# Optimization experiments

Hardware: AMD Instinct MI355X
Metric: run time of the kernel (lower is better)

The kernel has to match this reference:

```python
import jax, jax.numpy as jnp
import numpy as np

B, T, D_IN, H, C = 1024, 85, 20, 1024, 27
OBJ = T * 36  # flattened (T, 12, 3) object stream


def _mlp(h, W1, b1, W2, b2):
    # BaseEncoderDecoderLayout stand-in: Dense(H, relu) -> Dense(out)
    return jnp.maximum(h @ W1 + b1, 0.0) @ W2 + b2


def setup_inputs() -> dict:
    key = jax.random.key(0)
    ks = jax.random.split(key, 8)
    s = lambda k, shape: jax.random.normal(k, shape, jnp.float32) * 0.02
    return {
        "o": jax.random.normal(ks[0], (B, OBJ), jnp.float32),
        "x": jax.random.normal(ks[1], (B, T, D_IN), jnp.float32),
        # objProcess = BaseEncoderDecoderLayout(num_hid, dim_output=num_hid)
        "oW1": s(ks[2], (OBJ, H)), "ob1": jnp.zeros((H,), jnp.float32),
        "oW2": s(ks[3], (H, H)), "ob2": jnp.zeros((H,), jnp.float32),
        # expertWeightNet = BaseEncoderDecoderLayout(num_hid, dim_output=num_classes)
        "eW1": s(ks[4], (D_IN + H, H)), "eb1": jnp.zeros((H,), jnp.float32),
        "eW2": s(ks[5], (H, C)), "eb2": jnp.zeros((C,), jnp.float32),
    }


def reference(o, x, oW1, ob1, oW2, ob2, eW1, eb1, eW2, eb2):
    objInfo = _mlp(o, oW1, ob1, oW2, ob2)  # [B, H]

    def expert(cur):  # cur: [B, D_IN]
        return _mlp(jnp.concatenate([cur, objInfo], axis=-1), eW1, eb1, eW2, eb2)

    # step 0 uses raw x[:, 0, :]
    ew0 = expert(x[:, 0, :])  # [B, C]

    # steps 1..T-2: first feature of currentInput is replaced by previous
    # result's channel-0, i.e. result[:, -1, 0] -> sequential recurrence
    def step(prev, xt):  # prev: [B], xt: [B, D_IN]
        cur = jnp.concatenate([prev[:, None], xt[:, 1:]], axis=-1)
        ew = expert(cur)
        return ew[:, 0], ew

    xs = jnp.swapaxes(x[:, 1:T - 1, :], 0, 1)  # [T-2, B, D_IN]
    _, rest = jax.lax.scan(step, ew0[:, 0], xs)  # rest: [T-2, B, C]

    result = jnp.concatenate([ew0[None], rest], axis=0)  # [T-1, B, C]
    return jnp.swapaxes(result, 0, 1)  # [B, T-1, C]
```

## Files before the change

### kernel.cpp

```cpp
#include <hip/hip_runtime.h>
#include <hip/hip_bf16.h>

#define B_   1024
#define T_   85
#define DIN  20
#define H_   1024
#define C_   27
#define OBJ_ (T_ * 36)
#define TOUT (T_ - 1)

typedef unsigned short u16;
typedef __attribute__((ext_vector_type(8))) short bf16x8;
typedef __attribute__((ext_vector_type(4))) float f32x4;

__device__ __forceinline__ u16 f2bf(float f) {
    __hip_bfloat16 h = __float2bfloat16(f);
    return *reinterpret_cast<u16*>(&h);
}
__device__ __forceinline__ float bf2f(u16 u) {
    __hip_bfloat16 h;
    *reinterpret_cast<u16*>(&h) = u;
    return __bfloat162float(h);
}
__device__ __forceinline__ int f_as_i(float f) {
    union { float f; int i; } u; u.f = f; return u.i;
}
__device__ __forceinline__ float i_as_f(int i) {
    union { float f; int i; } u; u.i = i; return u.f;
}

__device__ __forceinline__ float wave64_sum_bcast(float p) {
    p += i_as_f(__builtin_amdgcn_update_dpp(0, f_as_i(p), 0x111, 0xf, 0xf, true));
    p += i_as_f(__builtin_amdgcn_update_dpp(0, f_as_i(p), 0x112, 0xf, 0xf, true));
    p += i_as_f(__builtin_amdgcn_update_dpp(0, f_as_i(p), 0x114, 0xf, 0xf, true));
    p += i_as_f(__builtin_amdgcn_update_dpp(0, f_as_i(p), 0x118, 0xf, 0xf, true));
    p += i_as_f(__builtin_amdgcn_update_dpp(0, f_as_i(p), 0x142, 0xa, 0xf, true));
    p += i_as_f(__builtin_amdgcn_update_dpp(0, f_as_i(p), 0x143, 0xc, 0xf, true));
    return i_as_f(__builtin_amdgcn_readlane(f_as_i(p), 63));
}

__global__ __launch_bounds__(256) void convertK2(
    const float* __restrict__ o, const float* __restrict__ oW1,
    const float* __restrict__ eW1, const float* __restrict__ oW2,
    const float* __restrict__ eW2, const float* __restrict__ ob2,
    u16* __restrict__ o_bf, u16* __restrict__ bW1t, u16* __restrict__ bE1t,
    u16* __restrict__ o2bf, u16* __restrict__ w2th,
    u16* __restrict__ e1t20, float* __restrict__ biasp)
{
    __shared__ float tl[64][65];
    const int bid = blockIdx.x, t = threadIdx.x;

    if (bid < 512) {
        for (int it = 0; it < 6; ++it) {
            const int idx = (bid * 256 + t) + it * 131072;
            const int row = idx / 768, g = idx - row * 768;
            float4 v = make_float4(0.f, 0.f, 0.f, 0.f);
            if (g < 765) v = *(const float4*)(o + (size_t)row * 3060 + g * 4);
            const float* vp = (const float*)&v;
            ushort4 uh;
            uh.x = f2bf(vp[0]); uh.y = f2bf(vp[1]);
            uh.z = f2bf(vp[2]); uh.w = f2bf(vp[3]);
            *(ushort4*)(o_bf + (size_t)row * 3072 + g * 4) = uh;
        }
    } else if (bid < 1536) {
        const bool isW1 = (bid < 1280);
        const int idx = isW1 ? (bid - 512) : (bid - 1280);
        const int k0 = (idx >> 4) * 64, n0 = (idx & 15) * 64;
        const float* src = isW1 ? oW1 : (eW1 + (size_t)DIN * H_);
        const int Ksrc = isW1 ? 3060 : 1024;
        u16* dst = isW1 ? bW1t : bE1t;
        const int ldk = isW1 ? 3072 : 1024;
#pragma unroll
        for (int r = 0; r < 4; ++r) {
            const int k = k0 + r * 16 + (t >> 4);
            float4 v = make_float4(0.f, 0.f, 0.f, 0.f);
            if (k < Ksrc)
                v = *(const float4*)(src + (size_t)k * 1024 + n0 + (t & 15) * 4);
            const float* vp = (const float*)&v;
#pragma unroll
            for (int j = 0; j < 4; ++j)
                tl[r * 16 + (t >> 4)][(t & 15) * 4 + j] = vp[j];
        }
        __syncthreads();
#pragma unroll
        for (int r = 0; r < 4; ++r) {
            const int n = r * 16 + (t >> 4);
            ushort4 u;
            u.x = f2bf(tl[(t & 15) * 4 + 0][n]);
            u.y = f2bf(tl[(t & 15) * 4 + 1][n]);
            u.z = f2bf(tl[(t & 15) * 4 + 2][n]);
            u.w = f2bf(tl[(t & 15) * 4 + 3][n]);
            *(ushort4*)(dst + (size_t)(n0 + n) * ldk + k0 + (t & 15) * 4) = u;
        }
    } else if (bid < 1664) {
        const int base = (bid - 1536) * 256 + t;
#pragma unroll
        for (int it = 0; it < 8; ++it) {
            const int g = base + it * 32768;
            float4 v = *(const float4*)(oW2 + (size_t)g * 4);
            const float* vp = (const float*)&v;
            ushort4 uh;
            uh.x = f2bf(vp[0]); uh.y = f2bf(vp[1]);
            uh.z = f2bf(vp[2]); uh.w = f2bf(vp[3]);
            *(ushort4*)(o2bf + (size_t)g * 4) = uh;
        }
    } else if (bid < 1696) {
        const int c = bid - 1664;
#pragma unroll
        for (int kk = 0; kk < 4; ++kk) {
            const int k = kk * 256 + t;
            const float v = (c < C_) ? eW2[(size_t)k * C_ + c] : 0.f;
            w2th[(size_t)c * 1024 + k] = f2bf(v);
        }
    } else if (bid < 1700) {
        const int n = (bid - 1696) * 256 + t;
        u16 buf[32];
#pragma unroll
        for (int k = 0; k < 32; ++k)
            buf[k] = (k < DIN) ? f2bf(eW1[(size_t)k * H_ + n]) : (u16)0;
#pragma unroll
        for (int q = 0; q < 4; ++q)
            *(uint4*)(e1t20 + (size_t)n * 32 + q * 8) = *(uint4*)&buf[q * 8];
    } else {
        const int r = bid - 1700, kc = r >> 2, nb = r & 3;
        const int n = nb * 256 + t;
        const int k0 = kc * 128;
        float acc = 0.f;
#pragma unroll 8
        for (int k = 0; k < 128; ++k)
            acc = fmaf(ob2[k0 + k], eW1[(size_t)(DIN + k0 + k) * H_ + n], acc);
        biasp[kc * H_ + n] = acc;
    }
}

template <int BN>
__device__ __forceinline__ void gemm_mfma_tile(
    const u16* __restrict__ A0, const u16* __restrict__ Bt,
    float* __restrict__ C, const float* __restrict__ bias,
    int ldK, int nk1, int gm0, int gn0, char* lds)
{
    constexpr int FN    = BN / 32;
    constexpr int WNw   = BN / 2;
    constexpr int BR    = BN / 64;
    constexpr int BUFSZ = 8192 + BN * 64;

    const int tid  = threadIdx.x;
    const int wave = tid >> 6, l = tid & 63, ml = l & 15, koct = l >> 4;
    const int wm = wave >> 1, wn = wave & 1;
    const int swz = koct ^ ((ml >> 1) & 3);
    const int a_ro = (wm * 64 + ml) * 64 + swz * 16;
    const int b_ro = (wn * WNw + ml) * 64 + swz * 16;

    const int sm = tid >> 2, sq = tid & 3;
    int wAo[2], wBo[BR];
    size_t gAo[2], gBo[BR];
#pragma unroll
    for (int q = 0; q < 2; ++q) {
        const int m = q * 64 + sm;
        wAo[q] = m * 64 + ((sq ^ ((m >> 1) & 3)) * 16);
        gAo[q] = (size_t)(gm0 + m) * ldK * 2 + sq * 16;
    }
#pragma unroll
    for (int q = 0; q < BR; ++q) {
        const int n = q * 64 + sm;
        wBo[q] = n * 64 + ((sq ^ ((n >> 1) & 3)) * 16);
        gBo[q] = (size_t)(gn0 + n) * ldK * 2 + sq * 16;
    }

    f32x4 acc[4][FN];
    const f32x4 zz = {0.f, 0.f, 0.f, 0.f};
#pragma unroll
    for (int i = 0; i < 4; ++i)
#pragma unroll
        for (int j = 0; j < FN; ++j) acc[i][j] = zz;

    const char* A0c = (const char*)A0;
    const char* Btc = (const char*)Bt;

    uint4 st[2 + BR];
    auto stage = [&](int kt) {
        const size_t koff = (size_t)kt * 64;
        st[0] = *(const uint4*)(A0c + gAo[0] + koff);
        st[1] = *(const uint4*)(A0c + gAo[1] + koff);
#pragma unroll
        for (int q = 0; q < BR; ++q)
            st[2 + q] = *(const uint4*)(Btc + gBo[q] + koff);
    };
    auto dswrite = [&](int buf) {
        char* d = lds + buf * BUFSZ;
        *(uint4*)(d + wAo[0]) = st[0];
        *(uint4*)(d + wAo[1]) = st[1];
#pragma unroll
        for (int q = 0; q < BR; ++q)
            *(uint4*)(d + 8192 + wBo[q]) = st[2 + q];
    };
    auto compute = [&](int buf) {
        const char* As = lds + buf * BUFSZ;
        const char* Bs = As + 8192;
        bf16x8 af[4], bfv[FN];
#pragma unroll
        for (int fm = 0; fm < 4; ++fm)
            af[fm] = *(const bf16x8*)(As + a_ro + fm * 1024);
#pragma unroll
        for (int fn = 0; fn < FN; ++fn)
            bfv[fn] = *(const bf16x8*)(Bs + b_ro + fn * 1024);
#pragma unroll
        for (int fm = 0; fm < 4; ++fm)
#pragma unroll
            for (int fn = 0; fn < FN; ++fn)
                acc[fm][fn] = __builtin_amdgcn_mfma_f32_16x16x32_bf16(
                    af[fm], bfv[fn], acc[fm][fn], 0, 0, 0);
    };

    stage(0); dswrite(0); __syncthreads();
    for (int kt = 0; kt < nk1; ++kt) {
        if (kt + 1 < nk1) stage(kt + 1);
        compute(kt & 1);
        if (kt + 1 < nk1) dswrite((kt + 1) & 1);
        __syncthreads();
    }

    float br[FN];
#pragma unroll
    for (int fn = 0; fn < FN; ++fn)
        br[fn] = bias ? bias[gn0 + wn * WNw + fn * 16 + ml] : 0.f;
#pragma unroll
    for (int fm = 0; fm < 4; ++fm) {
        const int rowb = gm0 + wm * 64 + fm * 16 + koct * 4;
#pragma unroll
        for (int fn = 0; fn < FN; ++fn) {
            const int col = gn0 + wn * WNw + fn * 16 + ml;
#pragma unroll
            for (int r = 0; r < 4; ++r)
                C[(size_t)(rowb + r) * 1024 + col] = acc[fm][fn][r] + br[fn];
        }
    }
}

__global__ __launch_bounds__(256) void kernelA2(
    const u16* __restrict__ o_bf, const u16* __restrict__ bW1t,
    const u16* __restrict__ o2bf, const u16* __restrict__ bE1t,
    float* __restrict__ p_h1, float* __restrict__ p_wc)
{
    __shared__ alignas(16) char lds[2 * 12288];
    const int bid = blockIdx.x;
    if (bid < 384) {
        const int c = bid >> 7, tl = bid & 127;
        gemm_mfma_tile<64>(o_bf + c * 1024, bW1t + c * 1024,
                           p_h1 + (size_t)c * 1048576, nullptr, 3072, 32,
                           (tl >> 4) * 128, (tl & 15) * 64, lds);
    } else {
        const int tl = bid - 384;
        gemm_mfma_tile<64>(o2bf, bE1t, p_wc, nullptr, 1024, 32,
                           (tl >> 4) * 128, (tl & 15) * 64, lds);
    }
}

__global__ __launch_bounds__(256) void epilogue2(
    const float* __restrict__ p_h1, const float* __restrict__ p_wc,
    const float* __restrict__ ob1, const float* __restrict__ eb1,
    const float* __restrict__ biasp,
    u16* __restrict__ h1bf, u16* __restrict__ Wct, float* __restrict__ biasWc)
{
    __shared__ float tl[64][65];
    const int bid = blockIdx.x, t = threadIdx.x;
    if (bid < 256) {
#pragma unroll
        for (int it = 0; it < 4; ++it) {
            const int g = bid * 1024 + it * 256 + t;
            const size_t e = (size_t)g * 4;
            float4 a = *(const float4*)(p_h1 + e);
            float4 b = *(const float4*)(p_h1 + 1048576 + e);
            float4 c = *(const float4*)(p_h1 + 2097152 + e);
            float4 s = *(const float4*)(ob1 + (e & 1023));
            const float *ap = (const float*)&a, *bp = (const float*)&b,
                        *cp = (const float*)&c, *sp = (const float*)&s;
            ushort4 uh;
            u16* up = (u16*)&uh;
#pragma unroll
            for (int j = 0; j < 4; ++j)
                up[j] = f2bf(fmaxf(ap[j] + bp[j] + cp[j] + sp[j], 0.f));
            *(ushort4*)(h1bf + e) = uh;
        }
    } else if (bid < 512) {
        const int idx = bid - 256;
        const int k0 = (idx >> 4) * 64, n0 = (idx & 15) * 64;
#pragma unroll
        for (int r = 0; r < 4; ++r) {
            const int k = k0 + r * 16 + (t >> 4);
            float4 v = *(const float4*)(p_wc + (size_t)k * 1024 + n0 + (t & 15) * 4);
            const float* vp = (const float*)&v;
#pragma unroll
            for (int j = 0; j < 4; ++j)
                tl[r * 16 + (t >> 4)][(t & 15) * 4 + j] = vp[j];
        }
        __syncthreads();
#pragma unroll
        for (int r = 0; r < 4; ++r) {
            const int n = r * 16 + (t >> 4);
            ushort4 u;
            u.x = f2bf(tl[(t & 15) * 4 + 0][n]);
            u.y = f2bf(tl[(t & 15) * 4 + 1][n]);
            u.z = f2bf(tl[(t & 15) * 4 + 2][n]);
            u.w = f2bf(tl[(t & 15) * 4 + 3][n]);
            *(ushort4*)(Wct + (size_t)(n0 + n) * 1024 + k0 + (t & 15) * 4) = u;
        }
    } else {
        const int j0 = t * 4;
        float4 s = *(const float4*)(eb1 + j0);
        float* sp = (float*)&s;
#pragma unroll
        for (int kc = 0; kc < 8; ++kc) {
            float4 p = *(const float4*)(biasp + kc * H_ + j0);
            const float* pp = (const float*)&p;
#pragma unroll
            for (int i = 0; i < 4; ++i) sp[i] += pp[i];
        }
        *(float4*)(biasWc + j0) = s;
    }
}

__global__ __launch_bounds__(256) void kernelB2(
    const u16* __restrict__ h1bf, const u16* __restrict__ Wct,
    const float* __restrict__ biasWc,
    float* __restrict__ base0, float* __restrict__ base1)
{
    __shared__ alignas(16) char lds[2 * 12288];
    const int bid = blockIdx.x;
    const int p = bid >> 7, tl = bid & 127;
    gemm_mfma_tile<64>(h1bf + p * 512, Wct + p * 512,
                       p ? base1 : base0, p ? biasWc : nullptr,
                       1024, 16, (tl >> 4) * 128, (tl & 15) * 64, lds);
}

#define CPH 16
#define CNPH 6

__global__ __launch_bounds__(64) void chain_seq4(
    const float* __restrict__ x, const u16* __restrict__ e1t20,
    const float* __restrict__ eW1, const float* __restrict__ eW2,
    const float* __restrict__ eb2,
    const float* __restrict__ base0, const float* __restrict__ base1,
    float* __restrict__ cur0_buf)
{
    __shared__ u16   A_bf[CPH * 1032];
    __shared__ float base_s[1024];
    __shared__ u16   xstage[16 * 32];

    const int b = blockIdx.x, l = threadIdx.x;
    const int ml = l & 15, koct = l >> 4;

#pragma unroll
    for (int i = 0; i < 16; ++i) {
        const int j = i * 64 + l;
        base_s[j] = base0[(size_t)b * H_ + j] + base1[(size_t)b * H_ + j];
    }
    float u[16], v[16];
#pragma unroll
    for (int i = 0; i < 16; ++i) {
        const int j = i * 64 + l;
        u[i] = eW1[j];
        v[i] = eW2[(size_t)j * C_];
    }
    const float eb20 = eb2[0];
    const float cur0_init = x[(size_t)b * (T_ * DIN)];
    float* cb = cur0_buf + (size_t)b * TOUT;

    const f32x4 zz = {0.f, 0.f, 0.f, 0.f};
    float prev = 0.f;
    int t = 0;

#pragma unroll 1
    for (int ph = 0; ph < CNPH; ++ph) {
        const int t0 = ph * CPH;

        {
            const int tr = l >> 2, kq = l & 3;
            const int tg = t0 + tr;
            u16 hw[8];
#pragma unroll
            for (int e = 0; e < 8; ++e) {
                const int k = kq * 8 + e;
                float vx = 0.f;
                if (k >= 1 && k < DIN && tg < T_)
                    vx = x[(size_t)b * (T_ * DIN) + tg * DIN + k];
                hw[e] = f2bf(vx);
            }
            uint4 pk;
            pk.x = hw[0] | ((unsigned)hw[1] << 16);
            pk.y = hw[2] | ((unsigned)hw[3] << 16);
            pk.z = hw[4] | ((unsigned)hw[5] << 16);
            pk.w = hw[6] | ((unsigned)hw[7] << 16);
            *(uint4*)&xstage[tr * 32 + kq * 8] = pk;
        }
        __syncthreads();

        {
            const bf16x8 af = *(const bf16x8*)&xstage[ml * 32 + koct * 8];
#pragma unroll 4
            for (int jt = 0; jt < 64; ++jt) {
                const bf16x8 bf = *(const bf16x8*)
                    &e1t20[(size_t)(jt * 16 + ml) * 32 + koct * 8];
                f32x4 c = __builtin_amdgcn_mfma_f32_16x16x32_bf16(
                    af, bf, zz, 0, 0, 0);
                const int jcol = jt * 16 + ml;
                const float bj = base_s[jcol];
#pragma unroll
                for (int r = 0; r < 4; ++r)
                    A_bf[(koct * 4 + r) * 1032 + jcol] = f2bf(c[r] + bj);
            }
        }
        __syncthreads();

        const int rem = 83 - t0;
        const int nst = (rem < CPH) ? rem : CPH;

        float a_cur[16];
#pragma unroll
        for (int i = 0; i < 16; ++i)
            a_cur[i] = bf2f(A_bf[i * 64 + l]);

        for (int sl = 0; sl < nst; ++sl, ++t) {
            const int sln = (sl + 1 < nst) ? sl + 1 : sl;
            float a_nxt[16];
#pragma unroll
            for (int i = 0; i < 16; ++i)
                a_nxt[i] = bf2f(A_bf[sln * 1032 + i * 64 + l]);

            const float cur0 = (t == 0) ? cur0_init : prev;
            if (l == 0) cb[t] = cur0;

            float p0 = 0.f, p1 = 0.f, p2 = 0.f, p3 = 0.f;
#pragma unroll
            for (int i = 0; i < 16; i += 4) {
                p0 = fmaf(fmaxf(fmaf(cur0, u[i + 0], a_cur[i + 0]), 0.f), v[i + 0], p0);
                p1 = fmaf(fmaxf(fmaf(cur0, u[i + 1], a_cur[i + 1]), 0.f), v[i + 1], p1);
                p2 = fmaf(fmaxf(fmaf(cur0, u[i + 2], a_cur[i + 2]), 0.f), v[i + 2], p2);
                p3 = fmaf(fmaxf(fmaf(cur0, u[i + 3], a_cur[i + 3]), 0.f), v[i + 3], p3);
            }
            const float p = (p0 + p1) + (p2 + p3);
            prev = eb20 + wave64_sum_bcast(p);

#pragma unroll
            for (int i = 0; i < 16; ++i) a_cur[i] = a_nxt[i];
        }
        __syncthreads();
    }
    if (l == 0) cb[TOUT - 1] = prev;
}

__global__ __launch_bounds__(256, 4) void expand(
    const float* __restrict__ x, const float* __restrict__ base0,
    const float* __restrict__ base1, const float* __restrict__ cur0_buf,
    const u16* __restrict__ e1t20, const u16* __restrict__ w2th,
    const float* __restrict__ eb2, float* __restrict__ out)
{
    __shared__ u16 A_lds[64 * 32];
    __shared__ u16 e_lds[128 * 32];
    __shared__ u16 h_lds[64 * 128];
    __shared__ u16 w2_s[32 * 128];
    __shared__ float base_s[2 * 128];

    const int tid = threadIdx.x;
    const int g0 = blockIdx.x * 64;
    const int w = tid >> 6, l = tid & 63, ml = l & 15, koct = l >> 4;
    const int b0 = g0 / 84;
    const int b1 = (b0 + 1 < B_) ? b0 + 1 : b0;

    {
        const int row = tid >> 2, q = tid & 3;
        const int g = g0 + row, bb = g / 84, tt = g - bb * 84;
        u16 hw[8];
#pragma unroll
        for (int c = 0; c < 8; ++c) {
            const int k = q * 8 + c;
            float v = 0.f;
            if (k == 0) v = cur0_buf[g];
            else if (k < DIN) v = x[(size_t)bb * (T_ * DIN) + tt * DIN + k];
            hw[c] = f2bf(v);
        }
        uint4 pk;
        pk.x = hw[0] | ((unsigned)hw[1] << 16);
        pk.y = hw[2] | ((unsigned)hw[3] << 16);
        pk.z = hw[4] | ((unsigned)hw[5] << 16);
        pk.w = hw[6] | ((unsigned)hw[7] << 16);
        *(uint4*)&A_lds[row * 32 + q * 8] = pk;
    }

    const int grow = w * 16 + ml;
    const int g = g0 + grow;
    const int sel = g / 84 - b0;
    __syncthreads();
    const bf16x8 xfrag = *(const bf16x8*)&A_lds[grow * 32 + koct * 8];

    f32x4 acc[2];
    const f32x4 zz = {0.f, 0.f, 0.f, 0.f};
    acc[0] = zz; acc[1] = zz;

#pragma unroll 1
    for (int kc = 0; kc < 8; ++kc) {
        const int n0 = kc * 128;
        if (kc) __syncthreads();
        {
            const u16* src = e1t20 + n0 * 32 + tid * 16;
            *(uint4*)&e_lds[tid * 16]     = *(const uint4*)src;
            *(uint4*)&e_lds[tid * 16 + 8] = *(const uint4*)(src + 8);
        }
        {
            const int wr = tid >> 3, sg = tid & 7;
            const u16* srcw = w2th + (size_t)wr * 1024 + n0 + sg * 16;
            const int s0 = (sg * 2) ^ (wr & 15), s1 = (sg * 2 + 1) ^ (wr & 15);
            *(uint4*)&w2_s[wr * 128 + s0 * 8] = *(const uint4*)srcw;
            *(uint4*)&w2_s[wr * 128 + s1 * 8] = *(const uint4*)(srcw + 8);
        }
        {
            const int bs = tid >> 7, c = tid & 127;
            const size_t rb = (size_t)(bs ? b1 : b0) * H_ + n0 + c;
            base_s[bs * 128 + c] = base0[rb] + base1[rb];
        }
        __syncthreads();

#pragma unroll
        for (int p = 0; p < 8; ++p) {
            const bf16x8 ef = *(const bf16x8*)&e_lds[(p * 16 + ml) * 32 + koct * 8];
            f32x4 c1 = zz;
            c1 = __builtin_amdgcn_mfma_f32_16x16x32_bf16(ef, xfrag, c1, 0, 0, 0);
            u16 hq[4];
#pragma unroll
            for (int q = 0; q < 4; ++q) {
                const int j = p * 16 + koct * 4 + q;
                const float v = c1[q] + base_s[sel * 128 + j];
                hq[q] = f2bf(fmaxf(v, 0.f));
            }
            uint2 pk;
            pk.x = hq[0] | ((unsigned)hq[1] << 16);
            pk.y = hq[2] | ((unsigned)hq[3] << 16);
            const int s16 = (p * 2 + (koct >> 1)) ^ ml;
            *(uint2*)&h_lds[grow * 128 + s16 * 8 + (koct & 1) * 4] = pk;
        }

#pragma unroll
        for (int ks = 0; ks < 4; ++ks) {
            const int sl = (((ks * 4 + koct) ^ ml)) * 8;
            const bf16x8 hf = *(const bf16x8*)&h_lds[grow * 128 + sl];
#pragma unroll
            for (int ct = 0; ct < 2; ++ct) {
                const bf16x8 wf = *(const bf16x8*)&w2_s[(ct * 16 + ml) * 128 + sl];
                acc[ct] = __builtin_amdgcn_mfma_f32_16x16x32_bf16(
                    wf, hf, acc[ct], 0, 0, 0);
            }
        }
    }

#pragma unroll
    for (int ct = 0; ct < 2; ++ct) {
#pragma unroll
        for (int q = 0; q < 4; ++q) {
            const int c = ct * 16 + koct * 4 + q;
            if (c < C_)
                out[(size_t)g * C_ + c] = acc[ct][q] + eb2[c];
        }
    }
}

struct GemmSmem {
    float As[2][16][68];
    float Bs[2][16][64];
};

template <int RELU>
__device__ __forceinline__ void gemm_core(
    const float* __restrict__ A, int lda,
    const float* __restrict__ Bm, int ldb,
    const float* __restrict__ bias, const float* __restrict__ bias_parts,
    float* __restrict__ Cc, int ldc, int K, int tile, GemmSmem& sm)
{
    const int tid = threadIdx.x;
    const int bm = (tile >> 4) * 64, bn = (tile & 15) * 64;
    const int wave = tid >> 6, l = tid & 63;
    const int n0 = (wave & 1) * 32 + (l & 7) * 4;
    const int m0 = (wave >> 1) * 32 + (l >> 3) * 4;
    const int am = tid >> 2, akq = tid & 3;
    const int bk = tid >> 4, bnq = tid & 15;
    const float* Arow = A + (size_t)(bm + am) * lda + akq * 4;
    const float* Brow = Bm + (size_t)bk * ldb + bn + bnq * 4;
    float acc[4][4] = {};
    const int nIter = (K + 15) >> 4;
    {
        const int ak = akq * 4;
        float4 av = (ak + 4 <= K) ? *(const float4*)(Arow)
                                  : make_float4(0.f, 0.f, 0.f, 0.f);
        float4 bv = (bk < K) ? *(const float4*)(Brow)
                             : make_float4(0.f, 0.f, 0.f, 0.f);
        sm.As[0][akq * 4 + 0][am] = av.x; sm.As[0][akq * 4 + 1][am] = av.y;
        sm.As[0][akq * 4 + 2][am] = av.z; sm.As[0][akq * 4 + 3][am] = av.w;
        *(float4*)&sm.Bs[0][bk][bnq * 4] = bv;
    }
    __syncthreads();
    for (int it = 0; it < nIter; ++it) {
        const int cur = it & 1;
        const bool pf = (it + 1 < nIter);
        float4 pav, pbv;
        if (pf) {
            const int k0 = (it + 1) << 4, ak = k0 + akq * 4;
            pav = (ak + 4 <= K) ? *(const float4*)(Arow + k0)
                                : make_float4(0.f, 0.f, 0.f, 0.f);
            pbv = (k0 + bk < K) ? *(const float4*)(Brow + (size_t)k0 * ldb)
                                : make_float4(0.f, 0.f, 0.f, 0.f);
        }
#pragma unroll
        for (int kk = 0; kk < 16; ++kk) {
            float ar[4], br[4];
            *(float4*)ar = *(const float4*)&sm.As[cur][kk][m0];
            *(float4*)br = *(const float4*)&sm.Bs[cur][kk][n0];
#pragma unroll
            for (int r = 0; r < 4; ++r)
#pragma unroll
                for (int c = 0; c < 4; ++c)
                    acc[r][c] = fmaf(ar[r], br[c], acc[r][c]);
        }
        if (pf) {
            const int nb = cur ^ 1;
            sm.As[nb][akq * 4 + 0][am] = pav.x; sm.As[nb][akq * 4 + 1][am] = pav.y;
            sm.As[nb][akq * 4 + 2][am] = pav.z; sm.As[nb][akq * 4 + 3][am] = pav.w;
            *(float4*)&sm.Bs[nb][bk][bnq * 4] = pbv;
        }
        __syncthreads();
    }
    float bias4[4];
#pragma unroll
    for (int c = 0; c < 4; ++c) {
        const int col = bn + n0 + c;
        float b = bias ? bias[col] : 0.f;
        if (bias_parts)
#pragma unroll
            for (int p = 0; p < 8; ++p) b += bias_parts[p * H_ + col];
        bias4[c] = b;
    }
#pragma unroll
    for (int r = 0; r < 4; ++r) {
        float4 v; float* vp = (float*)&v;
#pragma unroll
        for (int c = 0; c < 4; ++c) {
            float t2 = acc[r][c] + bias4[c];
            if (RELU) t2 = fmaxf(t2, 0.f);
            vp[c] = t2;
        }
        *(float4*)&Cc[(size_t)(bm + m0 + r) * ldc + bn + n0] = v;
    }
}

__global__ __launch_bounds__(256) void kernelA_fb(
    const float* __restrict__ o, const float* __restrict__ oW1,
    const float* __restrict__ ob1, const float* __restrict__ oW2,
    const float* __restrict__ eW1, const float* __restrict__ ob2,
    float* __restrict__ h1, float* __restrict__ Wc, float* __restrict__ biasc)
{
    __shared__ GemmSmem sm;
    const int bid = blockIdx.x;
    if (bid < 256) {
        gemm_core<1>(o, OBJ_, oW1, H_, ob1, nullptr, h1, H_, OBJ_, bid, sm);
    } else if (bid < 512) {
        gemm_core<0>(oW2, H_, eW1 + (size_t)DIN * H_, H_, nullptr, nullptr,
                     Wc, H_, H_, bid - 256, sm);
    } else {
        const int r = bid - 512, kc = r >> 2, nb = r & 3;
        const int n = nb * 256 + (int)threadIdx.x;
        const int k0 = kc * 128;
        float acc = 0.f;
#pragma unroll 8
        for (int k = 0; k < 128; ++k)
            acc = fmaf(ob2[k0 + k], eW1[(size_t)(DIN + k0 + k) * H_ + n], acc);
        biasc[kc * H_ + n] = acc;
    }
}

__global__ __launch_bounds__(256) void kernelB_fb(
    const float* __restrict__ h1, const float* __restrict__ Wc,
    const float* __restrict__ eb1, const float* __restrict__ biasc,
    float* __restrict__ base0)
{
    __shared__ GemmSmem sm;
    gemm_core<0>(h1, H_, Wc, H_, eb1, biasc, base0, H_, H_, blockIdx.x, sm);
}

__global__ __launch_bounds__(256, 2) void expert_seq_fb(
    const float* __restrict__ x, const float* __restrict__ eW1,
    const float* __restrict__ eW2, const float* __restrict__ eb2,
    const float* __restrict__ base0, float* __restrict__ out)
{
    const int b   = blockIdx.x;
    const int tid = threadIdx.x;
    const int j0  = tid * 4;

    __shared__ float xl[T_ * DIN];
    __shared__ float pl[256 * 29];
    __shared__ float pl2[256];
    __shared__ float prevs;

    for (int idx = tid; idx < T_ * DIN; idx += 256)
        xl[idx] = x[(size_t)b * (T_ * DIN) + idx];

    float w1r[DIN][4];
#pragma unroll
    for (int d = 0; d < DIN; ++d)
        *(float4*)w1r[d] = *(const float4*)&eW1[(size_t)d * H_ + j0];

    float base_r[4];
    *(float4*)base_r = *(const float4*)&base0[(size_t)b * H_ + j0];

    float w2r[4][C_];
#pragma unroll
    for (int i = 0; i < 4; ++i)
#pragma unroll
        for (int c = 0; c < C_; ++c)
            w2r[i][c] = eW2[(size_t)(j0 + i) * C_ + c];

    const float myb = (tid < C_) ? eb2[tid] : 0.f;
    __syncthreads();

    float prev = 0.f;
#pragma unroll 1
    for (int t = 0; t < TOUT; ++t) {
        const float cur0 = (t == 0) ? xl[0] : prev;
        float h[4];
#pragma unroll
        for (int i = 0; i < 4; ++i)
            h[i] = fmaf(cur0, w1r[0][i], base_r[i]);
#pragma unroll
        for (int d = 1; d < DIN; ++d) {
            const float xv = xl[t * DIN + d];
#pragma unroll
            for (int i = 0; i < 4; ++i)
                h[i] = fmaf(xv, w1r[d][i], h[i]);
        }
#pragma unroll
        for (int i = 0; i < 4; ++i)
            h[i] = fmaxf(h[i], 0.f);
        float p[C_];
#pragma unroll
        for (int c = 0; c < C_; ++c)
            p[c] = h[0] * w2r[0][c];
#pragma unroll
        for (int i = 1; i < 4; ++i)
#pragma unroll
            for (int c = 0; c < C_; ++c)
                p[c] = fmaf(h[i], w2r[i][c], p[c]);
#pragma unroll
        for (int c = 0; c < C_; ++c)
            pl[tid * 29 + c] = p[c];
        __syncthreads();
        {
            const int c2 = tid & 31, grp = tid >> 5;
            float s = 0.f;
            if (c2 < C_) {
                const int basei = grp * 32 * 29 + c2;
#pragma unroll
                for (int s2 = 0; s2 < 32; ++s2)
                    s += pl[basei + s2 * 29];
            }
            pl2[tid] = s;
        }
        __syncthreads();
        if (tid < C_) {
            float o = myb;
#pragma unroll
            for (int g = 0; g < 8; ++g)
                o += pl2[g * 32 + tid];
            out[((size_t)b * TOUT + t) * C_ + tid] = o;
            if (tid == 0) prevs = o;
        }
        __syncthreads();
        prev = prevs;
    }
}

extern "C" void kernel_launch(void* const* d_in, const int* in_sizes, int n_in,
                              void* d_out, int out_size, void* d_ws, size_t ws_size,
                              hipStream_t stream)
{
    const float* o   = (const float*)d_in[0];
    const float* x   = (const float*)d_in[1];
    const float* oW1 = (const float*)d_in[2];
    const float* ob1 = (const float*)d_in[3];
    const float* oW2 = (const float*)d_in[4];
    const float* ob2 = (const float*)d_in[5];
    const float* eW1 = (const float*)d_in[6];
    const float* eb1 = (const float*)d_in[7];
    const float* eW2 = (const float*)d_in[8];
    const float* eb2 = (const float*)d_in[9];

    float* outp = (float*)d_out;
    float* ws   = (float*)d_ws;
    dim3 blk(256);

    const size_t NEED2 = 38326272;
    if (ws_size >= NEED2) {
        float* p_h1   = ws;
        float* p_wc   = ws + 3145728;
        float* biasWc = ws + 4194304;
        float* cur0b  = ws + 4195328;
        float* biasp  = ws + 4281344;
        u16*   ub     = (u16*)(ws + 4289536);
        u16 *o_bf  = ub,             *bW1t = ub + 3145728;
        u16 *bE1t  = ub + 6291456,   *o2bf = ub + 7340032;
        u16 *h1bf  = ub + 8388608,   *Wct  = ub + 9437184;
        u16 *w2th  = ub + 10485760;
        u16 *e1t20 = ub + 10551296;
        float* base0 = p_h1;
        float* base1 = p_h1 + 1048576;

        convertK2<<<dim3(1732), blk, 0, stream>>>(o, oW1, eW1, oW2, eW2, ob2,
                                                  o_bf, bW1t, bE1t, o2bf,
                                                  w2th, e1t20, biasp);
        kernelA2<<<dim3(512), blk, 0, stream>>>(o_bf, bW1t, o2bf, bE1t,
                                                p_h1, p_wc);
        epilogue2<<<dim3(513), blk, 0, stream>>>(p_h1, p_wc, ob1, eb1, biasp,
                                                 h1bf, Wct, biasWc);
        kernelB2<<<dim3(256), blk, 0, stream>>>(h1bf, Wct, biasWc,
                                                base0, base1);
        chain_seq4<<<dim3(B_), dim3(64), 0, stream>>>(x, e1t20, eW1, eW2, eb2,
                                                      base0, base1, cur0b);
        expand<<<dim3(1344), blk, 0, stream>>>(x, base0, base1, cur0b, e1t20,
                                               w2th, eb2, outp);
    } else {
        const size_t MF = (size_t)H_ * H_;
        float* h1    = ws;
        float* Wc    = ws + MF;
        float* base0 = ws + 2 * MF;
        float* biasc = outp;
        kernelA_fb<<<dim3(544), blk, 0, stream>>>(o, oW1, ob1, oW2, eW1, ob2,
                                                  h1, Wc, biasc);
        kernelB_fb<<<dim3(256), blk, 0, stream>>>(h1, Wc, eb1, biasc, base0);
        expert_seq_fb<<<dim3(B_), blk, 0, stream>>>(x, eW1, eW2, eb2,
                                                    base0, outp);
    }
}
```

Before: 166.1 us.

## Warp-specialize chain kernel: producer waves precompute next phase while one wave runs recurrence

The sequential chain kernel now runs 256 threads per block. Three producer waves compute the MFMA pre-activations for the next phase of 8 steps into a double-buffered LDS tile, while wave 0 runs the serial recurrence on the current phase. This hides the per-phase MFMA prologue behind the latency-bound recurrence. The costs are more barriers (11 phases instead of 6), a larger LDS footprint and block size that may lower occupancy, and producer work wasted on lanes whose output is discarded.

Result: no change. 165.7 us (-0.3%).

```diff
diff --git a/kernel.cpp b/kernel.cpp
--- a/kernel.cpp
+++ b/kernel.cpp
@@ -333,120 +333,138 @@
                        1024, 16, (tl >> 4) * 128, (tl & 15) * 64, lds);
 }
 
-#define CPH 16
-#define CNPH 6
-
-__global__ __launch_bounds__(64) void chain_seq4(
+#define CPH 8
+#define CNPH 11
+
+__global__ __launch_bounds__(256, 3) void chain_seq5(
     const float* __restrict__ x, const u16* __restrict__ e1t20,
     const float* __restrict__ eW1, const float* __restrict__ eW2,
     const float* __restrict__ eb2,
     const float* __restrict__ base0, const float* __restrict__ base1,
     float* __restrict__ cur0_buf)
 {
-    __shared__ u16   A_bf[CPH * 1032];
+    __shared__ u16   A_bf[2][CPH * 1032];
     __shared__ float base_s[1024];
-    __shared__ u16   xstage[16 * 32];
-
-    const int b = blockIdx.x, l = threadIdx.x;
+
+    const int b = blockIdx.x, tid = threadIdx.x;
+    const int w = tid >> 6, l = tid & 63;
     const int ml = l & 15, koct = l >> 4;
 
-#pragma unroll
-    for (int i = 0; i < 16; ++i) {
-        const int j = i * 64 + l;
-        base_s[j] = base0[(size_t)b * H_ + j] + base1[(size_t)b * H_ + j];
-    }
-    float u[16], v[16];
-#pragma unroll
-    for (int i = 0; i < 16; ++i) {
-        const int j = i * 64 + l;
-        u[i] = eW1[j];
-        v[i] = eW2[(size_t)j * C_];
-    }
-    const float eb20 = eb2[0];
-    const float cur0_init = x[(size_t)b * (T_ * DIN)];
-    float* cb = cur0_buf + (size_t)b * TOUT;
+    {
+        const int j = tid * 4;
+        float4 b0v = *(const float4*)&base0[(size_t)b * H_ + j];
+        float4 b1v = *(const float4*)&base1[(size_t)b * H_ + j];
+        float4 s;
+        s.x = b0v.x + b1v.x; s.y = b0v.y + b1v.y;
+        s.z = b0v.z + b1v.z; s.w = b0v.w + b1v.w;
+        *(float4*)&base_s[j] = s;
+    }
+    __syncthreads();
 
     const f32x4 zz = {0.f, 0.f, 0.f, 0.f};
-    float prev = 0.f;
-    int t = 0;
-
-#pragma unroll 1
-    for (int ph = 0; ph < CNPH; ++ph) {
+
+    auto produce = [&](int ph) {
         const int t0 = ph * CPH;
-
+        u16 hw[8];
+        const int tg = t0 + ml;
+        const bool rowok = (ml < CPH) && (tg < T_);
+#pragma unroll
+        for (int e = 0; e < 8; ++e) {
+            const int k = koct * 8 + e;
+            float vx = 0.f;
+            if (rowok && k >= 1 && k < DIN)
+                vx = x[(size_t)b * (T_ * DIN) + tg * DIN + k];
+            hw[e] = f2bf(vx);
+        }
+        bf16x8 af;
         {
-            const int tr = l >> 2, kq = l & 3;
-            const int tg = t0 + tr;
-            u16 hw[8];
-#pragma unroll
-            for (int e = 0; e < 8; ++e) {
-                const int k = kq * 8 + e;
-                float vx = 0.f;
-                if (k >= 1 && k < DIN && tg < T_)
-                    vx = x[(size_t)b * (T_ * DIN) + tg * DIN + k];
-                hw[e] = f2bf(vx);
-            }
             uint4 pk;
             pk.x = hw[0] | ((unsigned)hw[1] << 16);
             pk.y = hw[2] | ((unsigned)hw[3] << 16);
             pk.z = hw[4] | ((unsigned)hw[5] << 16);
             pk.w = hw[6] | ((unsigned)hw[7] << 16);
-            *(uint4*)&xstage[tr * 32 + kq * 8] = pk;
-        }
-        __syncthreads();
-
-        {
-            const bf16x8 af = *(const bf16x8*)&xstage[ml * 32 + koct * 8];
-#pragma unroll 4
-            for (int jt = 0; jt < 64; ++jt) {
-                const bf16x8 bf = *(const bf16x8*)
-                    &e1t20[(size_t)(jt * 16 + ml) * 32 + koct * 8];
-                f32x4 c = __builtin_amdgcn_mfma_f32_16x16x32_bf16(
-                    af, bf, zz, 0, 0, 0);
+            af = *(bf16x8*)&pk;
+        }
+        const int beg = (w == 1) ? 0 : (w == 2) ? 22 : 43;
+        const int end = (w == 1) ? 22 : (w == 2) ? 43 : 64;
+        u16* dst = A_bf[ph & 1];
+#pragma unroll 2
+        for (int jt = beg; jt < end; ++jt) {
+            const bf16x8 bf = *(const bf16x8*)
+                &e1t20[(size_t)(jt * 16 + ml) * 32 + koct * 8];
+            f32x4 c = __builtin_amdgcn_mfma_f32_16x16x32_bf16(af, bf, zz, 0, 0, 0);
+            if (koct < 2) {
                 const int jcol = jt * 16 + ml;
                 const float bj = base_s[jcol];
 #pragma unroll
                 for (int r = 0; r < 4; ++r)
-                    A_bf[(koct * 4 + r) * 1032 + jcol] = f2bf(c[r] + bj);
+                    dst[(koct * 4 + r) * 1032 + jcol] = f2bf(c[r] + bj);
             }
         }
+    };
+
+    float u[16], v[16];
+    float prev = 0.f, cur0_init = 0.f;
+    if (w) {
+        produce(0);
+    } else {
+#pragma unroll
+        for (int i = 0; i < 16; ++i) {
+            const int j = i * 64 + l;
+            u[i] = eW1[j];
+            v[i] = eW2[(size_t)j * C_];
+        }
+        cur0_init = x[(size_t)b * (T_ * DIN)];
+    }
+    __syncthreads();
+
+    const float eb20 = eb2[0];
+    float* cb = cur0_buf + (size_t)b * TOUT;
+
+#pragma unroll 1
+    for (int ph = 0; ph < CNPH; ++ph) {
+        if (w) {
+            if (ph + 1 < CNPH) produce(ph + 1);
+        } else {
+            const int t0 = ph * CPH;
+            const int rem = 83 - t0;
+            const int nst = (rem < CPH) ? rem : CPH;
+            const u16* Abuf = A_bf[ph & 1];
+
+            float a_cur[16];
+#pragma unroll
+            for (int i = 0; i < 16; ++i)
+                a_cur[i] = bf2f(Abuf[i * 64 + l]);
+
+            for (int sl = 0; sl < nst; ++sl) {
+                const int t = t0 + sl;
+                const int sln = (sl + 1 < nst) ? sl + 1 : sl;
+                float a_nxt[16];
+#pragma unroll
+                for (int i = 0; i < 16; ++i)
+                    a_nxt[i] = bf2f(Abuf[sln * 1032 + i * 64 + l]);
+
+                const float cur0 = (t == 0) ? cur0_init : prev;
+                if (l == 0) cb[t] = cur0;
+
+                float p0 = 0.f, p1 = 0.f, p2 = 0.f, p3 = 0.f;
+#pragma unroll
+                for (int i = 0; i < 16; i += 4) {
+                    p0 = fmaf(fmaxf(fmaf(cur0, u[i + 0], a_cur[i + 0]), 0.f), v[i + 0], p0);
+                    p1 = fmaf(fmaxf(fmaf(cur0, u[i + 1], a_cur[i + 1]), 0.f), v[i + 1], p1);
+                    p2 = fmaf(fmaxf(fmaf(cur0, u[i + 2], a_cur[i + 2]), 0.f), v[i + 2], p2);
+                    p3 = fmaf(fmaxf(fmaf(cur0, u[i + 3], a_cur[i + 3]), 0.f), v[i + 3], p3);
+                }
+                const float p = (p0 + p1) + (p2 + p3);
+                prev = eb20 + wave64_sum_bcast(p);
+
+#pragma unroll
+                for (int i = 0; i < 16; ++i) a_cur[i] = a_nxt[i];
+            }
+        }
         __syncthreads();
-
-        const int rem = 83 - t0;
-        const int nst = (rem < CPH) ? rem : CPH;
-
-        float a_cur[16];
-#pragma unroll
-        for (int i = 0; i < 16; ++i)
-            a_cur[i] = bf2f(A_bf[i * 64 + l]);
-
-        for (int sl = 0; sl < nst; ++sl, ++t) {
-            const int sln = (sl + 1 < nst) ? sl + 1 : sl;
-            float a_nxt[16];
-#pragma unroll
-            for (int i = 0; i < 16; ++i)
-                a_nxt[i] = bf2f(A_bf[sln * 1032 + i * 64 + l]);
-
-            const float cur0 = (t == 0) ? cur0_init : prev;
-            if (l == 0) cb[t] = cur0;
-
-            float p0 = 0.f, p1 = 0.f, p2 = 0.f, p3 = 0.f;
-#pragma unroll
-            for (int i = 0; i < 16; i += 4) {
-                p0 = fmaf(fmaxf(fmaf(cur0, u[i + 0], a_cur[i + 0]), 0.f), v[i + 0], p0);
-                p1 = fmaf(fmaxf(fmaf(cur0, u[i + 1], a_cur[i + 1]), 0.f), v[i + 1], p1);
-                p2 = fmaf(fmaxf(fmaf(cur0, u[i + 2], a_cur[i + 2]), 0.f), v[i + 2], p2);
-                p3 = fmaf(fmaxf(fmaf(cur0, u[i + 3], a_cur[i + 3]), 0.f), v[i + 3], p3);
-            }
-            const float p = (p0 + p1) + (p2 + p3);
-            prev = eb20 + wave64_sum_bcast(p);
-
-#pragma unroll
-            for (int i = 0; i < 16; ++i) a_cur[i] = a_nxt[i];
-        }
-        __syncthreads();
-    }
-    if (l == 0) cb[TOUT - 1] = prev;
+    }
+    if (w == 0 && l == 0) cb[TOUT - 1] = prev;
 }
 
 __global__ __launch_bounds__(256, 4) void expand(
@@ -819,8 +837,8 @@
                                                  h1bf, Wct, biasWc);
         kernelB2<<<dim3(256), blk, 0, stream>>>(h1bf, Wct, biasWc,
                                                 base0, base1);
-        chain_seq4<<<dim3(B_), dim3(64), 0, stream>>>(x, e1t20, eW1, eW2, eb2,
-                                                      base0, base1, cur0b);
+        chain_seq5<<<dim3(B_), blk, 0, stream>>>(x, e1t20, eW1, eW2, eb2,
+                                                 base0, base1, cur0b);
         expand<<<dim3(1344), blk, 0, stream>>>(x, base0, base1, cur0b, e1t20,
                                                w2th, eb2, outp);
     } else {
```
